# Optimization experiments

Hardware: AMD Instinct MI355X
Metric: run time of the kernel (lower is better)

## Reference

```python
import jax, jax.numpy as jnp
import numpy as np

DIM = 768
HEADS = 12
HEAD_DIM = DIM // HEADS
HIDDEN = int(DIM * 4.0)
EPS = 1e-5


def _layernorm(x, g, b):
    mu = jnp.mean(x, axis=-1, keepdims=True)
    var = jnp.var(x, axis=-1, keepdims=True)
    return (x - mu) * jax.lax.rsqrt(var + EPS) * g + b


def setup_inputs() -> dict:
    key = jax.random.key(0)
    ks = jax.random.split(key, 12)
    s = 0.02
    return {
        "x": jax.random.normal(ks[0], (8, 1024, DIM), dtype=jnp.float32),
        "norm1_g": jnp.ones((DIM,), jnp.float32),
        "norm1_b": jnp.zeros((DIM,), jnp.float32),
        "qkv_w": jax.random.normal(ks[1], (3 * DIM, DIM), jnp.float32) * s,
        "qkv_b": jnp.zeros((3 * DIM,), jnp.float32),
        "proj_w": jax.random.normal(ks[2], (DIM, DIM), jnp.float32) * s,
        "proj_b": jnp.zeros((DIM,), jnp.float32),
        "norm2_g": jnp.ones((DIM,), jnp.float32),
        "norm2_b": jnp.zeros((DIM,), jnp.float32),
        "fc1_w": jax.random.normal(ks[3], (HIDDEN, DIM), jnp.float32) * s,
        "fc1_b": jnp.zeros((HIDDEN,), jnp.float32),
        "fc2_w": jax.random.normal(ks[4], (DIM, HIDDEN), jnp.float32) * s,
        "fc2_b": jnp.zeros((DIM,), jnp.float32),
    }


def reference(x, norm1_g, norm1_b, qkv_w, qkv_b, proj_w, proj_b,
              norm2_g, norm2_b, fc1_w, fc1_b, fc2_w, fc2_b):
    B, N, C = x.shape
    scale = HEAD_DIM ** -0.5

    # --- MHSA with pre-norm + residual ---
    h = _layernorm(x, norm1_g, norm1_b)
    qkv = h @ qkv_w.T + qkv_b                      # [B, N, 3C]
    qkv = qkv.reshape(B, N, 3, HEADS, HEAD_DIM)
    qkv = jnp.transpose(qkv, (2, 0, 3, 1, 4))      # [3, B, H, N, Dh]
    q, k, v = qkv[0], qkv[1], qkv[2]
    attn = jnp.einsum("bhnd,bhmd->bhnm", q, k) * scale
    attn = jax.nn.softmax(attn, axis=-1)
    o = jnp.einsum("bhnm,bhmd->bhnd", attn, v)     # [B, H, N, Dh]
    o = jnp.transpose(o, (0, 2, 1, 3)).reshape(B, N, C)
    x = x + (o @ proj_w.T + proj_b)

    # --- MLP with pre-norm + residual ---
    h = _layernorm(x, norm2_g, norm2_b)
    h = jax.nn.gelu(h @ fc1_w.T + fc1_b, approximate=False)
    x = x + (h @ fc2_w.T + fc2_b)
    return x
```

## Files before the change

### kernel.cpp

```cpp
#include <hip/hip_runtime.h>
#include <hip/hip_bf16.h>

typedef unsigned short u16;
using short8  = __attribute__((ext_vector_type(8))) short;
using floatx4 = __attribute__((ext_vector_type(4))) float;

__device__ inline u16 f2bu(float f) {
    __hip_bfloat16 h = __float2bfloat16(f);
    return __builtin_bit_cast(u16, h);
}
__device__ inline float b2f(u16 u) {
    unsigned v = (unsigned)u << 16;
    return __builtin_bit_cast(float, v);
}
__device__ inline float gelu_f(float v) {
    float u = 1.5957691216f * (v + 0.044715f * v * v * v);
    return v / (1.f + __expf(-u));
}

__device__ inline void load16(const u16* g, u16* l) {
    __builtin_amdgcn_global_load_lds(
        (const __attribute__((address_space(1))) void*)g,
        (__attribute__((address_space(3))) void*)l, 16, 0, 0);
}

__global__ void cvt_bf16v(const float4* __restrict__ in, ushort4* __restrict__ out, int n4) {
    int i = blockIdx.x * 256 + threadIdx.x;
    if (i < n4) {
        float4 f = in[i];
        ushort4 r;
        r.x = f2bu(f.x); r.y = f2bu(f.y); r.z = f2bu(f.z); r.w = f2bu(f.w);
        out[i] = r;
    }
}

__global__ __launch_bounds__(256) void layernorm_bf16(
    const float* __restrict__ x, const float* __restrict__ g,
    const float* __restrict__ b, u16* __restrict__ out)
{
    int row = blockIdx.x;
    int tid = threadIdx.x;
    const float* xr = x + (size_t)row * 768;
    float v0 = xr[tid], v1 = xr[tid + 256], v2 = xr[tid + 512];
    float s = v0 + v1 + v2;
    float ss = v0 * v0 + v1 * v1 + v2 * v2;
    for (int off = 1; off < 64; off <<= 1) {
        s  += __shfl_xor(s, off, 64);
        ss += __shfl_xor(ss, off, 64);
    }
    __shared__ float as[4], ass[4];
    int wave = tid >> 6, lane = tid & 63;
    if (lane == 0) { as[wave] = s; ass[wave] = ss; }
    __syncthreads();
    s  = as[0] + as[1] + as[2] + as[3];
    ss = ass[0] + ass[1] + ass[2] + ass[3];
    float mu  = s * (1.0f / 768.0f);
    float var = ss * (1.0f / 768.0f) - mu * mu;
    float rs  = rsqrtf(var + 1e-5f);
    u16* orow = out + (size_t)row * 768;
    orow[tid]       = f2bu((v0 - mu) * rs * g[tid]       + b[tid]);
    orow[tid + 256] = f2bu((v1 - mu) * rs * g[tid + 256] + b[tid + 256]);
    orow[tid + 512] = f2bu((v2 - mu) * rs * g[tid + 512] + b[tid + 512]);
}

__global__ __launch_bounds__(256) void red2(
    const ushort4* __restrict__ P0, const ushort4* __restrict__ P1,
    const float* __restrict__ bias, const float4* __restrict__ res,
    float4* __restrict__ out)
{
    int i = blockIdx.x * 256 + threadIdx.x;
    int col = (i % 192) * 4;
    ushort4 a = P0[i], b = P1[i];
    float4 o = res ? res[i] : out[i];
    o.x += bias[col + 0] + b2f(a.x) + b2f(b.x);
    o.y += bias[col + 1] + b2f(a.y) + b2f(b.y);
    o.z += bias[col + 2] + b2f(a.z) + b2f(b.z);
    o.w += bias[col + 3] + b2f(a.w) + b2f(b.w);
    out[i] = o;
}

__global__ __launch_bounds__(256) void red2_ln(
    const u16* __restrict__ P0, const u16* __restrict__ P1,
    const float* __restrict__ bias, const float* __restrict__ x,
    float* __restrict__ out,
    const float* __restrict__ g, const float* __restrict__ bb,
    u16* __restrict__ h)
{
    int row = blockIdx.x;
    int tid = threadIdx.x;
    size_t base = (size_t)row * 768;
    float v[3];
    float s = 0.f, ss = 0.f;
    #pragma unroll
    for (int j = 0; j < 3; ++j) {
        int col = tid + j * 256;
        size_t idx = base + col;
        float o = x[idx] + bias[col] + b2f(P0[idx]) + b2f(P1[idx]);
        out[idx] = o;
        v[j] = o;
        s += o; ss += o * o;
    }
    for (int off = 1; off < 64; off <<= 1) {
        s  += __shfl_xor(s, off, 64);
        ss += __shfl_xor(ss, off, 64);
    }
    __shared__ float as[4], ass[4];
    int wave = tid >> 6, lane = tid & 63;
    if (lane == 0) { as[wave] = s; ass[wave] = ss; }
    __syncthreads();
    s  = as[0] + as[1] + as[2] + as[3];
    ss = ass[0] + ass[1] + ass[2] + ass[3];
    float mu  = s * (1.0f / 768.0f);
    float var = ss * (1.0f / 768.0f) - mu * mu;
    float rs  = rsqrtf(var + 1e-5f);
    #pragma unroll
    for (int j = 0; j < 3; ++j) {
        int col = tid + j * 256;
        h[base + col] = f2bu((v[j] - mu) * rs * g[col] + bb[col]);
    }
}

__global__ __launch_bounds__(512, 4) void gemm_k64(
    const u16* __restrict__ A, int lda,
    const u16* __restrict__ B, int ldb,
    int K,
    const float* __restrict__ bias,
    const float* __restrict__ res,
    float* __restrict__ outf, u16* __restrict__ outb,
    u16* __restrict__ parts, size_t pstride,
    int ldc, int act, int splits)
{
    __shared__ u16 lsa[128 * 64];
    __shared__ u16 lsb[128 * 64];

    int tid  = threadIdx.x;
    int wave = tid >> 6, lane = tid & 63;
    int quad = lane >> 4, l16 = lane & 15;
    int wrow = (wave >> 1) * 32;
    int wcol = (wave & 1) * 64;

    int gx = gridDim.x;
    int nblk = gx * gridDim.y;
    int flat = blockIdx.y * gx + blockIdx.x;
    int d = (flat & 7) * (nblk >> 3) + (flat >> 3);
    int m0 = (d / gx) * 128, n0 = (d % gx) * 128;

    int Kper = K / splits;
    int kbeg = blockIdx.z * Kper;

    floatx4 acc[2][4];
    #pragma unroll
    for (int i = 0; i < 2; ++i)
        #pragma unroll
        for (int j = 0; j < 4; ++j)
            acc[i][j] = (floatx4){0.f, 0.f, 0.f, 0.f};

    int rsub = lane >> 3;
    int gc   = (lane & 7) ^ rsub;
    const u16* gA[2];
    const u16* gB[2];
    #pragma unroll
    for (int j = 0; j < 2; ++j) {
        int r = (j * 8 + wave) * 8 + rsub;
        gA[j] = A + (size_t)(m0 + r) * lda + kbeg + gc * 8;
        gB[j] = B + (size_t)(n0 + r) * ldb + kbeg + gc * 8;
    }

    int xq0 = ((quad)     ^ (l16 & 7)) * 8;
    int xq1 = ((quad + 4) ^ (l16 & 7)) * 8;

    for (int k0 = 0; k0 < Kper; k0 += 64) {
        __syncthreads();
        #pragma unroll
        for (int j = 0; j < 2; ++j) { load16(gA[j], &lsa[(j * 8 + wave) * 512]); gA[j] += 64; }
        #pragma unroll
        for (int j = 0; j < 2; ++j) { load16(gB[j], &lsb[(j * 8 + wave) * 512]); gB[j] += 64; }
        __syncthreads();

        short8 af[2], bfr[4];
        #pragma unroll
        for (int rb = 0; rb < 2; ++rb) af[rb]  = *(const short8*)&lsa[(wrow + rb * 16 + l16) * 64 + xq0];
        #pragma unroll
        for (int cb = 0; cb < 4; ++cb) bfr[cb] = *(const short8*)&lsb[(wcol + cb * 16 + l16) * 64 + xq0];
        #pragma unroll
        for (int rb = 0; rb < 2; ++rb)
            #pragma unroll
            for (int cb = 0; cb < 4; ++cb)
                acc[rb][cb] = __builtin_amdgcn_mfma_f32_16x16x32_bf16(af[rb], bfr[cb], acc[rb][cb], 0, 0, 0);
        #pragma unroll
        for (int rb = 0; rb < 2; ++rb) af[rb]  = *(const short8*)&lsa[(wrow + rb * 16 + l16) * 64 + xq1];
        #pragma unroll
        for (int cb = 0; cb < 4; ++cb) bfr[cb] = *(const short8*)&lsb[(wcol + cb * 16 + l16) * 64 + xq1];
        #pragma unroll
        for (int rb = 0; rb < 2; ++rb)
            #pragma unroll
            for (int cb = 0; cb < 4; ++cb)
                acc[rb][cb] = __builtin_amdgcn_mfma_f32_16x16x32_bf16(af[rb], bfr[cb], acc[rb][cb], 0, 0, 0);
    }

    u16* pdst = (splits > 1) ? parts + (size_t)blockIdx.z * pstride : nullptr;
    #pragma unroll
    for (int rb = 0; rb < 2; ++rb)
        #pragma unroll
        for (int cb = 0; cb < 4; ++cb)
            #pragma unroll
            for (int r = 0; r < 4; ++r) {
                int row = m0 + wrow + rb * 16 + quad * 4 + r;
                int col = n0 + wcol + cb * 16 + l16;
                float v = acc[rb][cb][r];
                if (splits > 1) {
                    pdst[(size_t)row * ldc + col] = f2bu(v);
                } else {
                    v += bias[col];
                    if (res) v += res[(size_t)row * ldc + col];
                    if (act) v = gelu_f(v);
                    if (outf) outf[(size_t)row * ldc + col] = v;
                    else      outb[(size_t)row * ldc + col] = f2bu(v);
                }
            }
}

__global__ __launch_bounds__(256) void attn_fused(
    const u16* __restrict__ qkv, u16* __restrict__ o)
{
    const int N = 1024, C3 = 2304;
    int qb = blockIdx.x;
    int bh = blockIdx.y;
    int b = bh / 12, h = bh % 12;
    int tid = threadIdx.x, wave = tid >> 6, lane = tid & 63;
    int quad = lane >> 4, l16 = lane & 15;

    __shared__ u16 lk[64 * 64];
    __shared__ u16 lvt[64][72];
    __shared__ u16 lp[4][32][72];

    const size_t base = (size_t)b * N * C3;
    int q0 = qb * 128 + wave * 32;

    short8 qa[2][2];
    #pragma unroll
    for (int rb = 0; rb < 2; ++rb)
        #pragma unroll
        for (int ch = 0; ch < 2; ++ch)
            qa[rb][ch] = *(const short8*)&qkv[base + (size_t)(q0 + rb * 16 + l16) * C3 + h * 64 + ch * 32 + quad * 8];

    floatx4 oacc[2][4];
    #pragma unroll
    for (int i = 0; i < 2; ++i)
        #pragma unroll
        for (int j = 0; j < 4; ++j) oacc[i][j] = (floatx4){0.f, 0.f, 0.f, 0.f};
    float lsum[2][4] = {};

    for (int kt = 0; kt < N; kt += 64) {
        __syncthreads();
        #pragma unroll
        for (int i = 0; i < 2; ++i) {
            int idx = i * 2048 + wave * 512 + lane * 8;
            int r = idx >> 6;
            int gc = (lane & 7) ^ (r & 7);
            load16(&qkv[base + (size_t)(kt + r) * C3 + 768 + h * 64 + gc * 8], &lk[idx]);
        }
        {
            int key = tid & 63, dbase = (tid >> 6) * 16;
            const u16* vp = &qkv[base + (size_t)(kt + key) * C3 + 1536 + h * 64 + dbase];
            uint4 vv0 = *(const uint4*)vp;
            uint4 vv1 = *(const uint4*)(vp + 8);
            const u16* e0 = (const u16*)&vv0;
            const u16* e1 = (const u16*)&vv1;
            #pragma unroll
            for (int i = 0; i < 8; ++i) {
                lvt[dbase + i][key]     = e0[i];
                lvt[dbase + 8 + i][key] = e1[i];
            }
        }
        __syncthreads();

        #pragma unroll
        for (int kb = 0; kb < 4; ++kb) {
            int R = kb * 16 + l16;
            short8 b0 = *(short8*)&lk[R * 64 + ((quad ^ (R & 7)) * 8)];
            short8 b1 = *(short8*)&lk[R * 64 + (((quad + 4) ^ (R & 7)) * 8)];
            #pragma unroll
            for (int rb = 0; rb < 2; ++rb) {
                floatx4 c = (floatx4){0.f, 0.f, 0.f, 0.f};
                c = __builtin_amdgcn_mfma_f32_16x16x32_bf16(qa[rb][0], b0, c, 0, 0, 0);
                c = __builtin_amdgcn_mfma_f32_16x16x32_bf16(qa[rb][1], b1, c, 0, 0, 0);
                #pragma unroll
                for (int r = 0; r < 4; ++r) {
                    float p = __expf(c[r] * 0.125f);
                    lsum[rb][r] += p;
                    lp[wave][rb * 16 + quad * 4 + r][kb * 16 + l16] = f2bu(p);
                }
            }
        }

        short8 pa[2][2];
        #pragma unroll
        for (int rb = 0; rb < 2; ++rb) {
            pa[rb][0] = *(short8*)&lp[wave][rb * 16 + l16][quad * 8];
            pa[rb][1] = *(short8*)&lp[wave][rb * 16 + l16][32 + quad * 8];
        }
        #pragma unroll
        for (int db = 0; db < 4; ++db) {
            short8 vb0 = *(short8*)&lvt[db * 16 + l16][quad * 8];
            short8 vb1 = *(short8*)&lvt[db * 16 + l16][32 + quad * 8];
            #pragma unroll
            for (int rb = 0; rb < 2; ++rb) {
                oacc[rb][db] = __builtin_amdgcn_mfma_f32_16x16x32_bf16(pa[rb][0], vb0, oacc[rb][db], 0, 0, 0);
                oacc[rb][db] = __builtin_amdgcn_mfma_f32_16x16x32_bf16(pa[rb][1], vb1, oacc[rb][db], 0, 0, 0);
            }
        }
    }

    #pragma unroll
    for (int rb = 0; rb < 2; ++rb)
        #pragma unroll
        for (int r = 0; r < 4; ++r)
            for (int off = 1; off < 16; off <<= 1)
                lsum[rb][r] += __shfl_xor(lsum[rb][r], off, 64);

    #pragma unroll
    for (int rb = 0; rb < 2; ++rb)
        #pragma unroll
        for (int db = 0; db < 4; ++db)
            #pragma unroll
            for (int r = 0; r < 4; ++r) {
                int row = q0 + rb * 16 + quad * 4 + r;
                int col = h * 64 + db * 16 + l16;
                o[(size_t)(b * N + row) * 768 + col] = f2bu(oacc[rb][db][r] / lsum[rb][r]);
            }
}

extern "C" void kernel_launch(void* const* d_in, const int* in_sizes, int n_in,
                              void* d_out, int out_size, void* d_ws, size_t ws_size,
                              hipStream_t stream) {
    const float* x      = (const float*)d_in[0];
    const float* n1g    = (const float*)d_in[1];
    const float* n1b    = (const float*)d_in[2];
    const float* qkv_w  = (const float*)d_in[3];
    const float* qkv_b  = (const float*)d_in[4];
    const float* proj_w = (const float*)d_in[5];
    const float* proj_b = (const float*)d_in[6];
    const float* n2g    = (const float*)d_in[7];
    const float* n2b    = (const float*)d_in[8];
    const float* fc1_w  = (const float*)d_in[9];
    const float* fc1_b  = (const float*)d_in[10];
    const float* fc2_w  = (const float*)d_in[11];
    const float* fc2_b  = (const float*)d_in[12];
    float* out = (float*)d_out;

    const int T = 8192;
    char* ws = (char*)d_ws;
    u16* w_qkv  = (u16*)ws;               ws += (size_t)2304 * 768 * 2;
    u16* w_proj = (u16*)ws;               ws += (size_t)768 * 768 * 2;
    u16* w_fc1  = (u16*)ws;               ws += (size_t)3072 * 768 * 2;
    u16* w_fc2  = (u16*)ws;               ws += (size_t)768 * 3072 * 2;
    u16* h_buf  = (u16*)ws;               ws += (size_t)T * 768 * 2;
    u16* qkvbuf = (u16*)ws;               ws += (size_t)T * 2304 * 2;
    u16* o_buf  = (u16*)ws;               ws += (size_t)T * 768 * 2;
    u16* pbuf   = (u16*)ws;               ws += (size_t)T * 768 * 2;
    u16* fc1out = qkvbuf;
    bool do_split = (size_t)(ws - (char*)d_ws) <= ws_size;
    size_t pstr = (size_t)(pbuf - h_buf);

    cvt_bf16v<<<dim3(2304 * 768 / 4 / 256), 256, 0, stream>>>((const float4*)qkv_w,  (ushort4*)w_qkv,  2304 * 768 / 4);
    cvt_bf16v<<<dim3(768 * 768 / 4 / 256),  256, 0, stream>>>((const float4*)proj_w, (ushort4*)w_proj, 768 * 768 / 4);
    cvt_bf16v<<<dim3(3072 * 768 / 4 / 256), 256, 0, stream>>>((const float4*)fc1_w,  (ushort4*)w_fc1,  3072 * 768 / 4);
    cvt_bf16v<<<dim3(768 * 3072 / 4 / 256), 256, 0, stream>>>((const float4*)fc2_w,  (ushort4*)w_fc2,  768 * 3072 / 4);

    layernorm_bf16<<<dim3(T), 256, 0, stream>>>(x, n1g, n1b, h_buf);
    gemm_k64<<<dim3(2304 / 128, T / 128), 512, 0, stream>>>(
        h_buf, 768, w_qkv, 768, 768, qkv_b, nullptr, nullptr, qkvbuf, nullptr, 0, 2304, 0, 1);
    attn_fused<<<dim3(8, 96), 256, 0, stream>>>(qkvbuf, o_buf);
    if (do_split) {
        gemm_k64<<<dim3(768 / 128, T / 128, 2), 512, 0, stream>>>(
            o_buf, 768, w_proj, 768, 768, proj_b, nullptr, nullptr, nullptr,
            h_buf, pstr, 768, 0, 2);
        red2_ln<<<dim3(T), 256, 0, stream>>>(
            h_buf, pbuf, proj_b, x, out, n2g, n2b, h_buf);
    } else {
        gemm_k64<<<dim3(768 / 128, T / 128), 512, 0, stream>>>(
            o_buf, 768, w_proj, 768, 768, proj_b, x, out, nullptr, nullptr, 0, 768, 0, 1);
        layernorm_bf16<<<dim3(T), 256, 0, stream>>>(out, n2g, n2b, h_buf);
    }
    gemm_k64<<<dim3(3072 / 128, T / 128), 512, 0, stream>>>(
        h_buf, 768, w_fc1, 768, 768, fc1_b, nullptr, nullptr, fc1out, nullptr, 0, 3072, 1, 1);
    if (do_split) {
        gemm_k64<<<dim3(768 / 128, T / 128, 2), 512, 0, stream>>>(
            fc1out, 3072, w_fc2, 3072, 3072, fc2_b, nullptr, nullptr, nullptr,
            h_buf, pstr, 768, 0, 2);
        red2<<<dim3(T * 768 / 4 / 256), 256, 0, stream>>>(
            (const ushort4*)h_buf, (const ushort4*)pbuf, fc2_b, nullptr, (float4*)out);
    } else {
        gemm_k64<<<dim3(768 / 128, T / 128), 512, 0, stream>>>(
            fc1out, 3072, w_fc2, 3072, 3072, fc2_b, out, out, nullptr, nullptr, 0, 768, 0, 1);
    }
}
```

Baseline: 369.4 us.

## Double-buffer LDS tiles in GEMM to overlap global loads with MFMA

The GEMM kernel's shared-memory tiles become two buffers. The next K-tile is loaded asynchronously with global_load_lds while the current one is being computed, using explicit vmcnt waits and raw barriers. This is meant to hide global-memory latency that was previously exposed by the load/sync/compute sequence. LDS use doubles to 64KB per block, which may cut occupancy below the launch_bounds target of 4, and the vmcnt(4) count assumes exactly four outstanding loads per stage.

```diff
diff --git a/kernel.cpp b/kernel.cpp
--- a/kernel.cpp
+++ b/kernel.cpp
@@ -130,8 +130,8 @@
     u16* __restrict__ parts, size_t pstride,
     int ldc, int act, int splits)
 {
-    __shared__ u16 lsa[128 * 64];
-    __shared__ u16 lsb[128 * 64];
+    __shared__ u16 lsa[2][128 * 64];
+    __shared__ u16 lsb[2][128 * 64];
 
     int tid  = threadIdx.x;
     int wave = tid >> 6, lane = tid & 63;
@@ -147,6 +147,7 @@
 
     int Kper = K / splits;
     int kbeg = blockIdx.z * Kper;
+    int NT = Kper >> 6;
 
     floatx4 acc[2][4];
     #pragma unroll
@@ -169,34 +170,49 @@
     int xq0 = ((quad)     ^ (l16 & 7)) * 8;
     int xq1 = ((quad + 4) ^ (l16 & 7)) * 8;
 
-    for (int k0 = 0; k0 < Kper; k0 += 64) {
-        __syncthreads();
-        #pragma unroll
-        for (int j = 0; j < 2; ++j) { load16(gA[j], &lsa[(j * 8 + wave) * 512]); gA[j] += 64; }
-        #pragma unroll
-        for (int j = 0; j < 2; ++j) { load16(gB[j], &lsb[(j * 8 + wave) * 512]); gB[j] += 64; }
-        __syncthreads();
-
+#define STAGE(bf_) do { \
+    _Pragma("unroll") \
+    for (int j_ = 0; j_ < 2; ++j_) { load16(gA[j_], &lsa[bf_][(j_ * 8 + wave) * 512]); gA[j_] += 64; } \
+    _Pragma("unroll") \
+    for (int j_ = 0; j_ < 2; ++j_) { load16(gB[j_], &lsb[bf_][(j_ * 8 + wave) * 512]); gB[j_] += 64; } \
+} while (0)
+
+    STAGE(0);
+
+    for (int c = 0; c < NT; ++c) {
+        int bc = c & 1;
+        __builtin_amdgcn_s_barrier();
+        if (c + 1 < NT) {
+            STAGE(bc ^ 1);
+            asm volatile("s_waitcnt vmcnt(4)" ::: "memory");
+        } else {
+            asm volatile("s_waitcnt vmcnt(0)" ::: "memory");
+        }
+        __builtin_amdgcn_s_barrier();
+
+        const u16* la = lsa[bc];
+        const u16* lb = lsb[bc];
         short8 af[2], bfr[4];
         #pragma unroll
-        for (int rb = 0; rb < 2; ++rb) af[rb]  = *(const short8*)&lsa[(wrow + rb * 16 + l16) * 64 + xq0];
-        #pragma unroll
-        for (int cb = 0; cb < 4; ++cb) bfr[cb] = *(const short8*)&lsb[(wcol + cb * 16 + l16) * 64 + xq0];
+        for (int rb = 0; rb < 2; ++rb) af[rb]  = *(const short8*)&la[(wrow + rb * 16 + l16) * 64 + xq0];
+        #pragma unroll
+        for (int cb = 0; cb < 4; ++cb) bfr[cb] = *(const short8*)&lb[(wcol + cb * 16 + l16) * 64 + xq0];
         #pragma unroll
         for (int rb = 0; rb < 2; ++rb)
             #pragma unroll
             for (int cb = 0; cb < 4; ++cb)
                 acc[rb][cb] = __builtin_amdgcn_mfma_f32_16x16x32_bf16(af[rb], bfr[cb], acc[rb][cb], 0, 0, 0);
         #pragma unroll
-        for (int rb = 0; rb < 2; ++rb) af[rb]  = *(const short8*)&lsa[(wrow + rb * 16 + l16) * 64 + xq1];
-        #pragma unroll
-        for (int cb = 0; cb < 4; ++cb) bfr[cb] = *(const short8*)&lsb[(wcol + cb * 16 + l16) * 64 + xq1];
+        for (int rb = 0; rb < 2; ++rb) af[rb]  = *(const short8*)&la[(wrow + rb * 16 + l16) * 64 + xq1];
+        #pragma unroll
+        for (int cb = 0; cb < 4; ++cb) bfr[cb] = *(const short8*)&lb[(wcol + cb * 16 + l16) * 64 + xq1];
         #pragma unroll
         for (int rb = 0; rb < 2; ++rb)
             #pragma unroll
             for (int cb = 0; cb < 4; ++cb)
                 acc[rb][cb] = __builtin_amdgcn_mfma_f32_16x16x32_bf16(af[rb], bfr[cb], acc[rb][cb], 0, 0, 0);
     }
+#undef STAGE
 
     u16* pdst = (splits > 1) ? parts + (size_t)blockIdx.z * pstride : nullptr;
     #pragma unroll
```

Measured after the change: 391.4 us. 6.0% more time.
